# Kernel tuning notes

Hardware: AMD Instinct MI355X
Metric: run time of the kernel (lower is better)

## Reference

```python
import jax, jax.numpy as jnp
import numpy as np

EPS = 1e-12


def setup_inputs() -> dict:
    key = jax.random.key(0)
    k1, k2 = jax.random.split(key)
    ide_feats = jax.random.normal(k1, (4096, 256), dtype=jnp.float32)
    u_feats = jax.random.normal(k2, (16384, 256), dtype=jnp.float32)
    return {"ide_feats": ide_feats, "u_feats": u_feats}


def reference(ide_feats, u_feats):
    # euclidean_dist: sqrt(sum((x_i - y_j)^2) + eps) -> [N, M]
    # computed via the GEMM expansion to avoid the [N, M, D] intermediate
    x2 = jnp.sum(ide_feats * ide_feats, axis=-1)[:, None]   # [N, 1]
    y2 = jnp.sum(u_feats * u_feats, axis=-1)[None, :]       # [1, M]
    xy = jnp.einsum('nd,md->nm', ide_feats, u_feats)        # [N, M]
    d2 = jnp.maximum(x2 + y2 - 2.0 * xy, 0.0)
    dists = jnp.sqrt(d2 + EPS)                              # [N, M]
    d = jnp.mean(dists, axis=-1)                            # [N]
    # dist_loss: sum_{i,j} sqrt((d_i - d_j)^2 + eps)
    diff = d[:, None] - d[None, :]                          # [N, N]
    loss = jnp.sum(jnp.sqrt(diff * diff + EPS))
    return loss
```

## Files before the change

kernel.cpp:

```cpp
#include <hip/hip_runtime.h>
#include <hip/hip_bf16.h>
#include <cstdint>

#define N_IDE 4096
#define M_U   16384
#define D_DIM 256
#define EPSF  1e-12f
#define INV_M (1.0f / 16384.0f)

typedef _Float16 f16x8 __attribute__((ext_vector_type(8)));
typedef float    f32x4 __attribute__((ext_vector_type(4)));

__device__ __forceinline__ void gll16(const void* g, void* l) {
  __builtin_amdgcn_global_load_lds(
      (const __attribute__((address_space(1))) void*)(uintptr_t)g,
      (__attribute__((address_space(3))) void*)(uint32_t)(uintptr_t)l,
      16, 0, 0);
}

__device__ __forceinline__ unsigned short f2h_bits(float f) {
  _Float16 h = (_Float16)f;
  return __builtin_bit_cast(unsigned short, h);
}

__global__ __launch_bounds__(256) void k_conv(const float* __restrict__ ide,
                                              const float* __restrict__ u,
                                              unsigned short* __restrict__ Ah,
                                              unsigned short* __restrict__ Bh,
                                              float* __restrict__ x2,
                                              float* __restrict__ y2) {
  int gw = (blockIdx.x * 256 + threadIdx.x) >> 6;
  int l  = threadIdx.x & 63;
  const float4* src;
  ushort4* dst;
  float* nrm;
  if (gw < N_IDE) {
    src = (const float4*)(ide + (size_t)gw * D_DIM);
    dst = (ushort4*)(Ah + (size_t)gw * D_DIM);
    nrm = x2 + gw;
  } else {
    int r = gw - N_IDE;
    src = (const float4*)(u + (size_t)r * D_DIM);
    dst = (ushort4*)(Bh + (size_t)r * D_DIM);
    nrm = y2 + r;
  }
  float4 v = src[l];
  float s = v.x * v.x + v.y * v.y + v.z * v.z + v.w * v.w;
  ushort4 o;
  o.x = f2h_bits(v.x); o.y = f2h_bits(v.y);
  o.z = f2h_bits(v.z); o.w = f2h_bits(v.w);
  dst[l] = o;
#pragma unroll
  for (int m = 1; m <= 32; m <<= 1) s += __shfl_xor(s, m, 64);
  if (l == 0) *nrm = s;
}

#define SB_ELEMS (256 * 64)
__global__ __launch_bounds__(256, 1) void k_gemm(const unsigned short* __restrict__ Ah,
                                                 const unsigned short* __restrict__ Bh,
                                                 const float* __restrict__ x2,
                                                 const float* __restrict__ y2,
                                                 float* __restrict__ dsum) {
  __shared__ __align__(16) unsigned short sA[128 * 256];
  __shared__ __align__(16) unsigned short sB[2 * SB_ELEMS];

  const int t    = threadIdx.x;
  const int w    = t >> 6;
  const int l    = t & 63;
  const int wm   = w >> 1, wn = w & 1;
  const int lrow = l & 15;
  const int lhi  = l >> 4;
  const int bx   = blockIdx.x;
  const int by   = blockIdx.y;

#pragma unroll
  for (int i = 0; i < 16; ++i) {
    int L = i * 256 + t;
    int row = L >> 5;
    int p = L & 31;
    int c = (p & 24) | ((p & 7) ^ (row & 7));
    gll16(Ah + (size_t)(by * 128 + row) * D_DIM + c * 8,
          sA + (size_t)(i * 256 + w * 64) * 8);
  }

  auto stageB = [&](int cgi, int kt, int buf) {
    const unsigned short* src = Bh + (size_t)cgi * 256 * D_DIM + kt * 64;
#pragma unroll
    for (int j = 0; j < 8; ++j) {
      int L = j * 256 + t;
      int row = L >> 3;
      int c = (L & 7) ^ (row & 7);
      gll16(src + (size_t)row * D_DIM + c * 8,
            sB + (size_t)(buf * SB_ELEMS) + (size_t)(j * 256 + w * 64) * 8);
    }
  };

  stageB(bx, 0, 0);
  __syncthreads();

  int s = 0;
  for (int cg = 0; cg < 8; ++cg) {
    const int cgi = cg * 8 + bx;

    f32x4 acc[4][8];
#pragma unroll
    for (int mi = 0; mi < 4; ++mi)
#pragma unroll
      for (int ni = 0; ni < 8; ++ni)
        acc[mi][ni] = (f32x4){0.f, 0.f, 0.f, 0.f};

    for (int kt = 0; kt < 4; ++kt) {
      if (s + 1 < 32)
        stageB(((s + 1) >> 2) * 8 + bx, (s + 1) & 3, (s + 1) & 1);

      f16x8 af[4][2];
#pragma unroll
      for (int mi = 0; mi < 4; ++mi)
#pragma unroll
        for (int ks = 0; ks < 2; ++ks) {
          int arow = wm * 64 + mi * 16 + lrow;
          int ac   = kt * 8 + (((ks << 2) | lhi) ^ (lrow & 7));
          af[mi][ks] = *(const f16x8*)(sA + (size_t)(arow * 32 + ac) * 8);
        }

      const unsigned short* bbuf = sB + (size_t)(s & 1) * SB_ELEMS;
#pragma unroll
      for (int half = 0; half < 2; ++half) {
        f16x8 bf[4][2];
#pragma unroll
        for (int nj = 0; nj < 4; ++nj)
#pragma unroll
          for (int ks = 0; ks < 2; ++ks) {
            int ni   = half * 4 + nj;
            int brow = wn * 128 + ni * 16 + lrow;
            int bc   = ((ks << 2) | lhi) ^ (lrow & 7);
            bf[nj][ks] = *(const f16x8*)(bbuf + (size_t)(brow * 8 + bc) * 8);
          }
#pragma unroll
        for (int mi = 0; mi < 4; ++mi)
#pragma unroll
          for (int nj = 0; nj < 4; ++nj) {
            int ni = half * 4 + nj;
            acc[mi][ni] = __builtin_amdgcn_mfma_f32_16x16x32_f16(af[mi][0], bf[nj][0], acc[mi][ni], 0, 0, 0);
            acc[mi][ni] = __builtin_amdgcn_mfma_f32_16x16x32_f16(af[mi][1], bf[nj][1], acc[mi][ni], 0, 0, 0);
          }
      }
      __syncthreads();
      ++s;
    }

    float yv[8];
#pragma unroll
    for (int ni = 0; ni < 8; ++ni)
      yv[ni] = y2[cgi * 256 + wn * 128 + ni * 16 + lrow];

#pragma unroll
    for (int mi = 0; mi < 4; ++mi) {
#pragma unroll
      for (int rr = 0; rr < 4; ++rr) {
        int grow = by * 128 + wm * 64 + mi * 16 + lhi * 4 + rr;
        float xv = x2[grow];
        float ssum = 0.f;
#pragma unroll
        for (int ni = 0; ni < 8; ++ni) {
          float d2 = xv + yv[ni] - 2.0f * acc[mi][ni][rr];
          d2 = fmaxf(d2, 0.0f);
          ssum += __builtin_amdgcn_sqrtf(d2 + EPSF);
        }
        ssum += __shfl_xor(ssum, 1, 64);
        ssum += __shfl_xor(ssum, 2, 64);
        ssum += __shfl_xor(ssum, 4, 64);
        ssum += __shfl_xor(ssum, 8, 64);
        if (lrow == 0) atomicAdd(&dsum[grow], ssum);
      }
    }
  }
}

__global__ __launch_bounds__(256) void k_loss(const float* __restrict__ dsum,
                                              float* __restrict__ out) {
  __shared__ float sd[N_IDE];
  __shared__ float wsum[4];
  int t = threadIdx.x;
  for (int k = t; k < N_IDE; k += 256) sd[k] = dsum[k];
  __syncthreads();
  int tid = blockIdx.x * 256 + t;
  int i   = tid >> 4;
  int jl  = tid & 15;
  float di = sd[i];
  float s  = 0.f;
  for (int k = 0; k < 256; ++k) {
    float diff = (di - sd[jl + k * 16]) * INV_M;
    s += __builtin_amdgcn_sqrtf(diff * diff + EPSF);
  }
#pragma unroll
  for (int m = 1; m <= 32; m <<= 1) s += __shfl_xor(s, m, 64);
  if ((t & 63) == 0) wsum[t >> 6] = s;
  __syncthreads();
  if (t == 0) atomicAdd(out, wsum[0] + wsum[1] + wsum[2] + wsum[3]);
}

extern "C" void kernel_launch(void* const* d_in, const int* in_sizes, int n_in,
                              void* d_out, int out_size, void* d_ws, size_t ws_size,
                              hipStream_t stream) {
  (void)in_sizes; (void)n_in; (void)out_size; (void)ws_size;
  const float* ide = (const float*)d_in[0];
  const float* u   = (const float*)d_in[1];
  float* out = (float*)d_out;

  char* ws = (char*)d_ws;
  size_t off = 0;
  unsigned short* Ah = (unsigned short*)(ws + off); off += (size_t)N_IDE * D_DIM * 2;
  unsigned short* Bh = (unsigned short*)(ws + off); off += (size_t)M_U  * D_DIM * 2;
  float* x2   = (float*)(ws + off); off += (size_t)N_IDE * 4;
  float* y2   = (float*)(ws + off); off += (size_t)M_U * 4;
  float* dsum = (float*)(ws + off); off += (size_t)N_IDE * 4;

  hipMemsetAsync(d_out, 0, sizeof(float), stream);
  hipMemsetAsync(dsum, 0, (size_t)N_IDE * 4, stream);
  k_conv<<<(N_IDE + M_U) / 4, 256, 0, stream>>>(ide, u, Ah, Bh, x2, y2);
  k_gemm<<<dim3(8, 32), 256, 0, stream>>>(Ah, Bh, x2, y2, dsum);
  k_loss<<<256, 256, 0, stream>>>(dsum, out);
}
```

Before: 142.5 us.

## Widen GEMM block to 512 threads with 512-column B tiles and deterministic partial sums

```diff
diff --git a/kernel.cpp b/kernel.cpp
--- a/kernel.cpp
+++ b/kernel.cpp
@@ -7,6 +7,10 @@
 #define D_DIM 256
 #define EPSF  1e-12f
 #define INV_M (1.0f / 16384.0f)
+
+#define CGC   512
+#define BK    32
+#define SB_ELEMS (CGC * BK)
 
 typedef _Float16 f16x8 __attribute__((ext_vector_type(8)));
 typedef float    f32x4 __attribute__((ext_vector_type(4)));
@@ -55,51 +59,60 @@
   if (l == 0) *nrm = s;
 }
 
-#define SB_ELEMS (256 * 64)
-__global__ __launch_bounds__(256, 1) void k_gemm(const unsigned short* __restrict__ Ah,
+__global__ __launch_bounds__(512, 2) void k_gemm(const unsigned short* __restrict__ Ah,
                                                  const unsigned short* __restrict__ Bh,
                                                  const float* __restrict__ x2,
                                                  const float* __restrict__ y2,
-                                                 float* __restrict__ dsum) {
+                                                 float* __restrict__ partial) {
   __shared__ __align__(16) unsigned short sA[128 * 256];
   __shared__ __align__(16) unsigned short sB[2 * SB_ELEMS];
+  __shared__ float rowacc[4][128];
 
   const int t    = threadIdx.x;
   const int w    = t >> 6;
   const int l    = t & 63;
-  const int wm   = w >> 1, wn = w & 1;
+  const int wm   = w >> 2, wn = w & 3;
   const int lrow = l & 15;
   const int lhi  = l >> 4;
   const int bx   = blockIdx.x;
   const int by   = blockIdx.y;
 
-#pragma unroll
-  for (int i = 0; i < 16; ++i) {
-    int L = i * 256 + t;
+  rowacc[t >> 7][t & 127] = 0.f;
+
+#pragma unroll
+  for (int i = 0; i < 8; ++i) {
+    int L = i * 512 + t;
     int row = L >> 5;
     int p = L & 31;
     int c = (p & 24) | ((p & 7) ^ (row & 7));
     gll16(Ah + (size_t)(by * 128 + row) * D_DIM + c * 8,
-          sA + (size_t)(i * 256 + w * 64) * 8);
-  }
-
-  auto stageB = [&](int cgi, int kt, int buf) {
-    const unsigned short* src = Bh + (size_t)cgi * 256 * D_DIM + kt * 64;
-#pragma unroll
-    for (int j = 0; j < 8; ++j) {
-      int L = j * 256 + t;
-      int row = L >> 3;
-      int c = (L & 7) ^ (row & 7);
+          sA + (size_t)(i * 512 + w * 64) * 8);
+  }
+
+  auto stageB = [&](int s) {
+    const int cgi = (s >> 3) * 8 + bx;
+    const int kt  = s & 7;
+    const unsigned short* src = Bh + (size_t)cgi * CGC * D_DIM + kt * BK;
+    unsigned short* dstb = sB + (size_t)(s & 1) * SB_ELEMS;
+#pragma unroll
+    for (int j = 0; j < 4; ++j) {
+      int L = j * 512 + t;
+      int row = L >> 2;
+      int c = L & 3;
       gll16(src + (size_t)row * D_DIM + c * 8,
-            sB + (size_t)(buf * SB_ELEMS) + (size_t)(j * 256 + w * 64) * 8);
+            dstb + (size_t)(j * 512 + w * 64) * 8);
     }
   };
 
-  stageB(bx, 0, 0);
-  __syncthreads();
-
-  int s = 0;
-  for (int cg = 0; cg < 8; ++cg) {
+  float4 x2v[4];
+#pragma unroll
+  for (int mi = 0; mi < 4; ++mi)
+    x2v[mi] = *(const float4*)&x2[by * 128 + wm * 64 + mi * 16 + lhi * 4];
+
+  stageB(0);
+  __syncthreads();
+
+  for (int cg = 0; cg < 4; ++cg) {
     const int cgi = cg * 8 + bx;
 
     f32x4 acc[4][8];
@@ -109,61 +122,53 @@
       for (int ni = 0; ni < 8; ++ni)
         acc[mi][ni] = (f32x4){0.f, 0.f, 0.f, 0.f};
 
-    for (int kt = 0; kt < 4; ++kt) {
-      if (s + 1 < 32)
-        stageB(((s + 1) >> 2) * 8 + bx, (s + 1) & 3, (s + 1) & 1);
-
-      f16x8 af[4][2];
-#pragma unroll
-      for (int mi = 0; mi < 4; ++mi)
-#pragma unroll
-        for (int ks = 0; ks < 2; ++ks) {
-          int arow = wm * 64 + mi * 16 + lrow;
-          int ac   = kt * 8 + (((ks << 2) | lhi) ^ (lrow & 7));
-          af[mi][ks] = *(const f16x8*)(sA + (size_t)(arow * 32 + ac) * 8);
+    for (int kt = 0; kt < 8; ++kt) {
+      const int s = cg * 8 + kt;
+      if (s + 1 < 32) stageB(s + 1);
+
+      f16x8 af[4];
+#pragma unroll
+      for (int mi = 0; mi < 4; ++mi) {
+        int arow = wm * 64 + mi * 16 + lrow;
+        int lc   = kt * 4 + lhi;
+        int pc   = (lc & 24) | ((lc & 7) ^ (lrow & 7));
+        af[mi] = *(const f16x8*)(sA + (size_t)arow * 256 + pc * 8);
+      }
+
+      const unsigned short* bbuf = sB + (size_t)(s & 1) * SB_ELEMS;
+#pragma unroll
+      for (int half = 0; half < 2; ++half) {
+        f16x8 bf[4];
+#pragma unroll
+        for (int nj = 0; nj < 4; ++nj) {
+          int brow = wn * 128 + (half * 4 + nj) * 16 + lrow;
+          bf[nj] = *(const f16x8*)(bbuf + (size_t)brow * BK + lhi * 8);
         }
-
-      const unsigned short* bbuf = sB + (size_t)(s & 1) * SB_ELEMS;
-#pragma unroll
-      for (int half = 0; half < 2; ++half) {
-        f16x8 bf[4][2];
-#pragma unroll
-        for (int nj = 0; nj < 4; ++nj)
-#pragma unroll
-          for (int ks = 0; ks < 2; ++ks) {
-            int ni   = half * 4 + nj;
-            int brow = wn * 128 + ni * 16 + lrow;
-            int bc   = ((ks << 2) | lhi) ^ (lrow & 7);
-            bf[nj][ks] = *(const f16x8*)(bbuf + (size_t)(brow * 8 + bc) * 8);
-          }
 #pragma unroll
         for (int mi = 0; mi < 4; ++mi)
 #pragma unroll
-          for (int nj = 0; nj < 4; ++nj) {
-            int ni = half * 4 + nj;
-            acc[mi][ni] = __builtin_amdgcn_mfma_f32_16x16x32_f16(af[mi][0], bf[nj][0], acc[mi][ni], 0, 0, 0);
-            acc[mi][ni] = __builtin_amdgcn_mfma_f32_16x16x32_f16(af[mi][1], bf[nj][1], acc[mi][ni], 0, 0, 0);
-          }
+          for (int nj = 0; nj < 4; ++nj)
+            acc[mi][half * 4 + nj] =
+                __builtin_amdgcn_mfma_f32_16x16x32_f16(af[mi], bf[nj],
+                                                       acc[mi][half * 4 + nj], 0, 0, 0);
       }
       __syncthreads();
-      ++s;
     }
 
     float yv[8];
 #pragma unroll
     for (int ni = 0; ni < 8; ++ni)
-      yv[ni] = y2[cgi * 256 + wn * 128 + ni * 16 + lrow];
+      yv[ni] = y2[cgi * CGC + wn * 128 + ni * 16 + lrow];
 
 #pragma unroll
     for (int mi = 0; mi < 4; ++mi) {
+      float xr[4] = {x2v[mi].x, x2v[mi].y, x2v[mi].z, x2v[mi].w};
 #pragma unroll
       for (int rr = 0; rr < 4; ++rr) {
-        int grow = by * 128 + wm * 64 + mi * 16 + lhi * 4 + rr;
-        float xv = x2[grow];
         float ssum = 0.f;
 #pragma unroll
         for (int ni = 0; ni < 8; ++ni) {
-          float d2 = xv + yv[ni] - 2.0f * acc[mi][ni][rr];
+          float d2 = xr[rr] + yv[ni] - 2.0f * acc[mi][ni][rr];
           d2 = fmaxf(d2, 0.0f);
           ssum += __builtin_amdgcn_sqrtf(d2 + EPSF);
         }
@@ -171,18 +176,29 @@
         ssum += __shfl_xor(ssum, 2, 64);
         ssum += __shfl_xor(ssum, 4, 64);
         ssum += __shfl_xor(ssum, 8, 64);
-        if (lrow == 0) atomicAdd(&dsum[grow], ssum);
+        if (lrow == 0)
+          rowacc[wn][wm * 64 + mi * 16 + lhi * 4 + rr] += ssum;
       }
     }
   }
-}
-
-__global__ __launch_bounds__(256) void k_loss(const float* __restrict__ dsum,
+
+  __syncthreads();
+  if (t < 128)
+    partial[(size_t)bx * N_IDE + by * 128 + t] =
+        rowacc[0][t] + rowacc[1][t] + rowacc[2][t] + rowacc[3][t];
+}
+
+__global__ __launch_bounds__(256) void k_loss(const float* __restrict__ partial,
                                               float* __restrict__ out) {
   __shared__ float sd[N_IDE];
   __shared__ float wsum[4];
   int t = threadIdx.x;
-  for (int k = t; k < N_IDE; k += 256) sd[k] = dsum[k];
+  for (int k = t; k < N_IDE; k += 256) {
+    float s = 0.f;
+#pragma unroll
+    for (int b = 0; b < 8; ++b) s += partial[(size_t)b * N_IDE + k];
+    sd[k] = s;
+  }
   __syncthreads();
   int tid = blockIdx.x * 256 + t;
   int i   = tid >> 4;
@@ -212,13 +228,12 @@
   size_t off = 0;
   unsigned short* Ah = (unsigned short*)(ws + off); off += (size_t)N_IDE * D_DIM * 2;
   unsigned short* Bh = (unsigned short*)(ws + off); off += (size_t)M_U  * D_DIM * 2;
-  float* x2   = (float*)(ws + off); off += (size_t)N_IDE * 4;
-  float* y2   = (float*)(ws + off); off += (size_t)M_U * 4;
-  float* dsum = (float*)(ws + off); off += (size_t)N_IDE * 4;
+  float* x2      = (float*)(ws + off); off += (size_t)N_IDE * 4;
+  float* y2      = (float*)(ws + off); off += (size_t)M_U * 4;
+  float* partial = (float*)(ws + off); off += (size_t)8 * N_IDE * 4;
 
   hipMemsetAsync(d_out, 0, sizeof(float), stream);
-  hipMemsetAsync(dsum, 0, (size_t)N_IDE * 4, stream);
   k_conv<<<(N_IDE + M_U) / 4, 256, 0, stream>>>(ide, u, Ah, Bh, x2, y2);
-  k_gemm<<<dim3(8, 32), 256, 0, stream>>>(Ah, Bh, x2, y2, dsum);
-  k_loss<<<256, 256, 0, stream>>>(dsum, out);
-}
+  k_gemm<<<dim3(8, 32), 512, 0, stream>>>(Ah, Bh, x2, y2, partial);
+  k_loss<<<256, 256, 0, stream>>>(partial, out);
+}
```

After: 128.0 us. -10.2%, faster.
